# Kernel optimization log

Measured on AMD Instinct MI355X. Metric: run time of the kernel, lower is better.

The kernel has to match this reference:

```python
import jax, jax.numpy as jnp
import numpy as np

B, N, DH, DG, HID, K_STEPS, CURV = 256, 2048, 128, 256, 256, 2, 1.0
SC = CURV ** 0.5
SCALE = 1.0 / (DH ** 0.5)
LN_EPS = 1e-5


def _artanh(x):
    return jnp.arctanh(jnp.clip(x, -1.0 + 1e-5, 1.0 - 1e-5))


def logmap0(x, sc=SC):
    n = jnp.maximum(jnp.linalg.norm(x, axis=-1, keepdims=True), 1e-7)
    return x * (_artanh(sc * n) / (sc * n))


def expmap0(v, sc=SC):
    n = jnp.maximum(jnp.linalg.norm(v, axis=-1, keepdims=True), 1e-7)
    return v * (jnp.tanh(sc * n) / (sc * n))


def setup_inputs() -> dict:
    key = jax.random.key(0)
    ks = jax.random.split(key, 16)

    def lin(k, out_d, in_d):
        return (jax.random.normal(k, (out_d, in_d), jnp.float32) * (in_d ** -0.5))

    demo_hyp = expmap0(0.1 * jax.random.normal(ks[0], (B, N, DH), jnp.float32))
    rho_g = jax.random.normal(ks[1], (B, DG), jnp.float32)
    return {
        "demo_hyp": demo_hyp,
        "rho_g": rho_g,
        "seed_g_w": lin(ks[2], DH, DG),
        "seed_g_b": jnp.zeros((DH,), jnp.float32),
        "seed_d_w": lin(ks[3], DH, DH),
        "pool_wq_w": lin(ks[4], DH, DH),
        "pool_wk_w": lin(ks[5], DH, DH),
        "pool_wv_w": lin(ks[6], DH, DH),
        "q_u_w": lin(ks[7], DH, DH),
        "q_g_w": lin(ks[8], DH, DG),
        "q_g_b": jnp.zeros((DH,), jnp.float32),
        "kv_w": lin(ks[9], DH, DH),
        "mlp_w1": lin(ks[10], HID, DH),
        "mlp_b1": jnp.zeros((HID,), jnp.float32),
        "mlp_w2": lin(ks[11], DH, HID),
        "mlp_b2": jnp.zeros((DH,), jnp.float32),
        "ln_g": jnp.ones((DH,), jnp.float32),
        "ln_b": jnp.zeros((DH,), jnp.float32),
    }


def reference(demo_hyp, rho_g, seed_g_w, seed_g_b, seed_d_w,
              pool_wq_w, pool_wk_w, pool_wv_w, q_u_w, q_g_w, q_g_b,
              kv_w, mlp_w1, mlp_b1, mlp_w2, mlp_b2, ln_g, ln_b):
    demo_tan = logmap0(demo_hyp)                       # (B,N,Dh)

    # seed: attention-pool demos with rho_g query
    q_seed = rho_g @ seed_g_w.T + seed_g_b             # (B,Dh)
    qk = q_seed @ pool_wq_w.T                          # (B,Dh)
    Kp = demo_tan @ pool_wk_w.T                        # (B,N,Dh)
    a = jax.nn.softmax(jnp.einsum('bd,bnd->bn', qk, Kp) * SCALE, axis=-1)
    Vp = demo_tan @ pool_wv_w.T
    pooled = jnp.einsum('bn,bnd->bd', a, Vp)           # (B,Dh)
    u = expmap0(q_seed + pooled @ seed_d_w.T)

    for _ in range(K_STEPS):
        u_tan = logmap0(u)
        mu = jnp.mean(u_tan, axis=-1, keepdims=True)
        var = jnp.var(u_tan, axis=-1, keepdims=True)
        u_tan = (u_tan - mu) * jax.lax.rsqrt(var + LN_EPS) * ln_g + ln_b
        q = u_tan @ q_u_w.T + rho_g @ q_g_w.T + q_g_b
        Kmat = demo_tan @ kv_w.T                       # keys == values
        att = jax.nn.softmax(jnp.einsum('bd,bnd->bn', q, Kmat) * SCALE, axis=-1)
        delta = jnp.einsum('bn,bnd->bd', att, Kmat)
        upd = jax.nn.gelu(delta @ mlp_w1.T + mlp_b1, approximate=False) @ mlp_w2.T + mlp_b2
        u = expmap0(u_tan + upd)
    return u
```

## Files before the change

### kernel.cpp

```cpp
#include <hip/hip_runtime.h>
#include <cstddef>
#include <cstdint>

#define B 256
#define N 2048
#define DH 128
#define DG 256
#define HID 256
#define SPLITS 8
#define CHUNK (N / SPLITS)
#define KITER (CHUNK / 16)
#define SCALE 0.08838834764831845f
#define LN_EPS 1e-5f
#define TAN_NORM_MAX 6.2f


__device__ __forceinline__ float artanh_clip(float a) {
  a = fminf(a, 1.0f - 1e-5f);
  return 0.5f * __logf((1.0f + a) / (1.0f - a));
}

__device__ __forceinline__ float logmap_scale(float n2) {
  float nc = fmaxf(sqrtf(n2), 1e-7f);
  return artanh_clip(nc) / nc;
}

__device__ __forceinline__ float dotN(const float* __restrict__ wrow,
                                      const float* __restrict__ x, int n4) {
  const float4* a = (const float4*)wrow;
  const float4* bx = (const float4*)x;
  float s = 0.f;
  for (int j = 0; j < n4; ++j) {
    float4 u = a[j], v = bx[j];
    s += u.x * v.x + u.y * v.y + u.z * v.z + u.w * v.w;
  }
  return s;
}

__device__ __forceinline__ float blockSum128(float v, float* s_red) {
#pragma unroll
  for (int msk = 1; msk < 64; msk <<= 1) v += __shfl_xor(v, msk);
  if ((threadIdx.x & 63) == 0) s_red[threadIdx.x >> 6] = v;
  __syncthreads();
  float r = s_red[0] + s_red[1];
  __syncthreads();
  return r;
}

__device__ __forceinline__ float combine_partials(const float* __restrict__ partials,
                                                  int b, int tid) {
  const float* pb = partials + (size_t)b * SPLITS * (DH + 2);
  float L = 0.f, a = 0.f;
#pragma unroll
  for (int s = 0; s < SPLITS; ++s) {
    L += pb[s * (DH + 2) + DH];
    a += pb[s * (DH + 2) + tid];
  }
  return a / L;
}


__global__ void setup_pool_query(const float* __restrict__ rho,
                                 const float* __restrict__ seed_g_w,
                                 const float* __restrict__ seed_g_b,
                                 const float* __restrict__ pool_wq_w,
                                 const float* __restrict__ pool_wk_w,
                                 float* __restrict__ q_seed,
                                 float* __restrict__ qvec,
                                 float* __restrict__ mb) {
  const int b = blockIdx.x, tid = threadIdx.x;
  __shared__ __align__(16) float s_rho[DG];
  __shared__ __align__(16) float s_qs[DH];
  __shared__ __align__(16) float s_qk[DH];
  __shared__ float s_red[2];
  s_rho[tid] = rho[b * DG + tid];
  s_rho[tid + DH] = rho[b * DG + tid + DH];
  __syncthreads();
  float qs = seed_g_b[tid] + dotN(seed_g_w + (size_t)tid * DG, s_rho, DG / 4);
  q_seed[b * DH + tid] = qs;
  s_qs[tid] = qs;
  __syncthreads();
  float qk = dotN(pool_wq_w + (size_t)tid * DH, s_qs, DH / 4);
  s_qk[tid] = qk;
  __syncthreads();
  float qp = 0.f;
  for (int i = 0; i < DH; ++i) qp += pool_wk_w[i * DH + tid] * s_qk[i];
  qvec[b * DH + tid] = qp;
  float qn2 = blockSum128(qp * qp, s_red);
  if (tid == 0) mb[b] = SCALE * TAN_NORM_MAX * sqrtf(qn2);
}


__global__ __launch_bounds__(256, 6) void attn_pass(const float* __restrict__ demo,
                                                    const float* __restrict__ qvec,
                                                    const float* __restrict__ mb,
                                                    float* __restrict__ partials) {
  const int blk = blockIdx.x;
  const int b = blk >> 3;
  const int s = blk & 7;
  const int tid = threadIdx.x;
  const int w = tid >> 6;
  const int lane = tid & 63;
  const int il = lane & 31;
  const int half = lane >> 5;

  const float4 qv = *(const float4*)(qvec + b * DH + ((lane * 4) & 127));
  const float Mb = mb[b];
  const float* p0 = demo + ((size_t)b * N + (size_t)s * CHUNK + (size_t)(w * 2)) * DH + lane * 4;

  float la = 0.f, lb = 0.f;
  float4 aa = make_float4(0.f, 0.f, 0.f, 0.f);
  float4 ab = make_float4(0.f, 0.f, 0.f, 0.f);

  float4 xa = *(const float4*)(p0);
  float4 xb = *(const float4*)(p0 + 8 * DH);

  for (int k = 0; k < KITER; ++k) {
    float4 ca = xa, cb = xb;
    if (k + 1 < KITER) {
      const float* pn_ = p0 + (size_t)(k + 1) * 16 * DH;
      xa = *(const float4*)(pn_);
      xb = *(const float4*)(pn_ + 8 * DH);
    }
    {
      float n2 = ca.x * ca.x + ca.y * ca.y + ca.z * ca.z + ca.w * ca.w;
      float dd = qv.x * ca.x + qv.y * ca.y + qv.z * ca.z + qv.w * ca.w;
#pragma unroll
      for (int msk = 1; msk < 32; msk <<= 1) {
        n2 += __shfl_xor(n2, msk);
        dd += __shfl_xor(dd, msk);
      }
      float ts = logmap_scale(n2);
      float p = __expf(dd * ts * SCALE - Mb);
      la += p;
      float c = p * ts;
      aa.x += c * ca.x; aa.y += c * ca.y; aa.z += c * ca.z; aa.w += c * ca.w;
    }
    {
      float n2 = cb.x * cb.x + cb.y * cb.y + cb.z * cb.z + cb.w * cb.w;
      float dd = qv.x * cb.x + qv.y * cb.y + qv.z * cb.z + qv.w * cb.w;
#pragma unroll
      for (int msk = 1; msk < 32; msk <<= 1) {
        n2 += __shfl_xor(n2, msk);
        dd += __shfl_xor(dd, msk);
      }
      float ts = logmap_scale(n2);
      float p = __expf(dd * ts * SCALE - Mb);
      lb += p;
      float c = p * ts;
      ab.x += c * cb.x; ab.y += c * cb.y; ab.z += c * cb.z; ab.w += c * cb.w;
    }
  }

  float l = la + lb;
  float4 acc;
  acc.x = aa.x + ab.x; acc.y = aa.y + ab.y; acc.z = aa.z + ab.z; acc.w = aa.w + ab.w;
  acc.x += __shfl_xor(acc.x, 32);
  acc.y += __shfl_xor(acc.y, 32);
  acc.z += __shfl_xor(acc.z, 32);
  acc.w += __shfl_xor(acc.w, 32);
  l += __shfl_xor(l, 32);

  __shared__ __align__(16) float s_acc[4][DH];
  __shared__ float s_l[4];
  if (half == 0) *(float4*)&s_acc[w][il * 4] = acc;
  if (lane == 0) s_l[w] = l;
  __syncthreads();
  if (tid < DH) {
    float a = s_acc[0][tid] + s_acc[1][tid] + s_acc[2][tid] + s_acc[3][tid];
    float* p = partials + (size_t)blk * (DH + 2);
    p[tid] = a;
    if (tid == 0) p[DH] = s_l[0] + s_l[1] + s_l[2] + s_l[3];
  }
}


__global__ void trans_pool(const float* __restrict__ partials,
                           const float* __restrict__ q_seed,
                           const float* __restrict__ rho,
                           const float* __restrict__ pool_wv_w,
                           const float* __restrict__ seed_d_w,
                           const float* __restrict__ q_u_w,
                           const float* __restrict__ q_g_w,
                           const float* __restrict__ q_g_b,
                           const float* __restrict__ kv_w,
                           const float* __restrict__ ln_g,
                           const float* __restrict__ ln_b,
                           float* __restrict__ u_tan_out,
                           float* __restrict__ qvec_out,
                           float* __restrict__ mb) {
  const int b = blockIdx.x, tid = threadIdx.x;
  __shared__ __align__(16) float s_a[DH];
  __shared__ __align__(16) float s_b[DH];
  __shared__ __align__(16) float s_rho[DG];
  __shared__ float s_red[2];

  float w0 = combine_partials(partials, b, tid);
  s_a[tid] = w0;
  s_rho[tid] = rho[b * DG + tid];
  s_rho[tid + DH] = rho[b * DG + tid + DH];
  __syncthreads();
  float pooled = dotN(pool_wv_w + (size_t)tid * DH, s_a, DH / 4);
  s_b[tid] = pooled;
  __syncthreads();
  float v = q_seed[b * DH + tid] + dotN(seed_d_w + (size_t)tid * DH, s_b, DH / 4);
  float n2 = blockSum128(v * v, s_red);
  float nc = fmaxf(sqrtf(n2), 1e-7f);
  float u = v * (tanhf(nc) / nc);
  float nu2 = blockSum128(u * u, s_red);
  float nuc = fmaxf(sqrtf(nu2), 1e-7f);
  float ut = u * (artanh_clip(nuc) / nuc);
  float mu = blockSum128(ut, s_red) * (1.0f / DH);
  float d = ut - mu;
  float var = blockSum128(d * d, s_red) * (1.0f / DH);
  float y = d * rsqrtf(var + LN_EPS) * ln_g[tid] + ln_b[tid];
  u_tan_out[b * DH + tid] = y;
  s_a[tid] = y;
  __syncthreads();
  float q = q_g_b[tid] + dotN(q_u_w + (size_t)tid * DH, s_a, DH / 4) +
            dotN(q_g_w + (size_t)tid * DG, s_rho, DG / 4);
  s_b[tid] = q;
  __syncthreads();
  float qp = 0.f;
  for (int i = 0; i < DH; ++i) qp += kv_w[i * DH + tid] * s_b[i];
  qvec_out[b * DH + tid] = qp;
  float qn2 = blockSum128(qp * qp, s_red);
  if (tid == 0) mb[b] = SCALE * TAN_NORM_MAX * sqrtf(qn2);
}


__global__ void trans_iter(const float* __restrict__ partials,
                           const float* __restrict__ u_tan_in,
                           const float* __restrict__ rho,
                           const float* __restrict__ kv_w,
                           const float* __restrict__ mlp_w1,
                           const float* __restrict__ mlp_b1,
                           const float* __restrict__ mlp_w2,
                           const float* __restrict__ mlp_b2,
                           const float* __restrict__ q_u_w,
                           const float* __restrict__ q_g_w,
                           const float* __restrict__ q_g_b,
                           const float* __restrict__ ln_g,
                           const float* __restrict__ ln_b,
                           float* __restrict__ u_tan_out,
                           float* __restrict__ qvec_out,
                           float* __restrict__ mb,
                           float* __restrict__ out, int is_final) {
  const int b = blockIdx.x, tid = threadIdx.x;
  __shared__ __align__(16) float s_a[DH];
  __shared__ __align__(16) float s_b[DH];
  __shared__ __align__(16) float s_h[HID];
  __shared__ __align__(16) float s_rho[DG];
  __shared__ float s_red[2];

  float wv = combine_partials(partials, b, tid);
  s_a[tid] = wv;
  s_rho[tid] = rho[b * DG + tid];
  s_rho[tid + DH] = rho[b * DG + tid + DH];
  __syncthreads();
  float delta = dotN(kv_w + (size_t)tid * DH, s_a, DH / 4);
  s_b[tid] = delta;
  __syncthreads();
  float h0 = mlp_b1[tid] + dotN(mlp_w1 + (size_t)tid * DH, s_b, DH / 4);
  float h1 = mlp_b1[tid + DH] + dotN(mlp_w1 + (size_t)(tid + DH) * DH, s_b, DH / 4);
  s_h[tid] = 0.5f * h0 * (1.0f + erff(h0 * 0.70710678118654752f));
  s_h[tid + DH] = 0.5f * h1 * (1.0f + erff(h1 * 0.70710678118654752f));
  __syncthreads();
  float upd = mlp_b2[tid] + dotN(mlp_w2 + (size_t)tid * HID, s_h, HID / 4);
  float v = u_tan_in[b * DH + tid] + upd;
  float n2 = blockSum128(v * v, s_red);
  float nc = fmaxf(sqrtf(n2), 1e-7f);
  float u = v * (tanhf(nc) / nc);
  if (is_final) {
    out[b * DH + tid] = u;
    return;
  }
  float nu2 = blockSum128(u * u, s_red);
  float nuc = fmaxf(sqrtf(nu2), 1e-7f);
  float ut = u * (artanh_clip(nuc) / nuc);
  float mu = blockSum128(ut, s_red) * (1.0f / DH);
  float d = ut - mu;
  float var = blockSum128(d * d, s_red) * (1.0f / DH);
  float y = d * rsqrtf(var + LN_EPS) * ln_g[tid] + ln_b[tid];
  u_tan_out[b * DH + tid] = y;
  s_a[tid] = y;
  __syncthreads();
  float q = q_g_b[tid] + dotN(q_u_w + (size_t)tid * DH, s_a, DH / 4) +
            dotN(q_g_w + (size_t)tid * DG, s_rho, DG / 4);
  s_b[tid] = q;
  __syncthreads();
  float qp = 0.f;
  for (int i = 0; i < DH; ++i) qp += kv_w[i * DH + tid] * s_b[i];
  qvec_out[b * DH + tid] = qp;
  float qn2 = blockSum128(qp * qp, s_red);
  if (tid == 0) mb[b] = SCALE * TAN_NORM_MAX * sqrtf(qn2);
}


extern "C" void kernel_launch(void* const* d_in, const int* in_sizes, int n_in,
                              void* d_out, int out_size, void* d_ws, size_t ws_size,
                              hipStream_t stream) {
  const float* demo      = (const float*)d_in[0];
  const float* rho       = (const float*)d_in[1];
  const float* seed_g_w  = (const float*)d_in[2];
  const float* seed_g_b  = (const float*)d_in[3];
  const float* seed_d_w  = (const float*)d_in[4];
  const float* pool_wq_w = (const float*)d_in[5];
  const float* pool_wk_w = (const float*)d_in[6];
  const float* pool_wv_w = (const float*)d_in[7];
  const float* q_u_w     = (const float*)d_in[8];
  const float* q_g_w     = (const float*)d_in[9];
  const float* q_g_b     = (const float*)d_in[10];
  const float* kv_w      = (const float*)d_in[11];
  const float* mlp_w1    = (const float*)d_in[12];
  const float* mlp_b1    = (const float*)d_in[13];
  const float* mlp_w2    = (const float*)d_in[14];
  const float* mlp_b2    = (const float*)d_in[15];
  const float* ln_g      = (const float*)d_in[16];
  const float* ln_b      = (const float*)d_in[17];
  float* out = (float*)d_out;

  float* ws = (float*)d_ws;
  float* qvec  = ws;
  float* qseed = ws + B * DH;
  float* utanA = ws + 2 * B * DH;
  float* utanB = ws + 3 * B * DH;
  float* mb    = ws + 4 * B * DH;
  float* parts = ws + 4 * B * DH + B;

  setup_pool_query<<<B, DH, 0, stream>>>(rho, seed_g_w, seed_g_b, pool_wq_w,
                                         pool_wk_w, qseed, qvec, mb);
  attn_pass<<<B * SPLITS, 256, 0, stream>>>(demo, qvec, mb, parts);
  trans_pool<<<B, DH, 0, stream>>>(parts, qseed, rho, pool_wv_w, seed_d_w,
                                   q_u_w, q_g_w, q_g_b, kv_w, ln_g, ln_b,
                                   utanA, qvec, mb);
  attn_pass<<<B * SPLITS, 256, 0, stream>>>(demo, qvec, mb, parts);
  trans_iter<<<B, DH, 0, stream>>>(parts, utanA, rho, kv_w, mlp_w1, mlp_b1,
                                   mlp_w2, mlp_b2, q_u_w, q_g_w, q_g_b, ln_g,
                                   ln_b, utanB, qvec, mb, out, 0);
  attn_pass<<<B * SPLITS, 256, 0, stream>>>(demo, qvec, mb, parts);
  trans_iter<<<B, DH, 0, stream>>>(parts, utanB, rho, kv_w, mlp_w1, mlp_b1,
                                   mlp_w2, mlp_b2, q_u_w, q_g_w, q_g_b, ln_g,
                                   ln_b, utanB, qvec, mb, out, 1);
}
```

Measured before the change: 615.6 us.

## Cache per-row logmap scales and use DPP 16-lane row reductions in attention pass

New measurement: 602.8 us. -2.1%, faster.

```diff
diff --git a/kernel.cpp b/kernel.cpp
--- a/kernel.cpp
+++ b/kernel.cpp
@@ -9,7 +9,8 @@
 #define HID 256
 #define SPLITS 8
 #define CHUNK (N / SPLITS)
-#define KITER (CHUNK / 16)
+#define ROWS_PER_ITER 32
+#define KITER (CHUNK / ROWS_PER_ITER)
 #define SCALE 0.08838834764831845f
 #define LN_EPS 1e-5f
 #define TAN_NORM_MAX 6.2f
@@ -23,6 +24,14 @@
 __device__ __forceinline__ float logmap_scale(float n2) {
   float nc = fmaxf(sqrtf(n2), 1e-7f);
   return artanh_clip(nc) / nc;
+}
+
+__device__ __forceinline__ float row16_sum(float x) {
+  x += __int_as_float(__builtin_amdgcn_update_dpp(0, __float_as_int(x), 0x128, 0xF, 0xF, true));
+  x += __int_as_float(__builtin_amdgcn_update_dpp(0, __float_as_int(x), 0x124, 0xF, 0xF, true));
+  x += __int_as_float(__builtin_amdgcn_update_dpp(0, __float_as_int(x), 0x122, 0xF, 0xF, true));
+  x += __int_as_float(__builtin_amdgcn_update_dpp(0, __float_as_int(x), 0x121, 0xF, 0xF, true));
+  return x;
 }
 
 __device__ __forceinline__ float dotN(const float* __restrict__ wrow,
@@ -91,86 +100,115 @@
 }
 
 
+template <int LOADTS>
 __global__ __launch_bounds__(256, 6) void attn_pass(const float* __restrict__ demo,
                                                     const float* __restrict__ qvec,
                                                     const float* __restrict__ mb,
-                                                    float* __restrict__ partials) {
+                                                    float* __restrict__ partials,
+                                                    float* __restrict__ ts_buf) {
   const int blk = blockIdx.x;
   const int b = blk >> 3;
   const int s = blk & 7;
   const int tid = threadIdx.x;
   const int w = tid >> 6;
   const int lane = tid & 63;
-  const int il = lane & 31;
-  const int half = lane >> 5;
-
-  const float4 qv = *(const float4*)(qvec + b * DH + ((lane * 4) & 127));
+  const int g = lane >> 4;
+  const int il = lane & 15;
+
+  const float4 qv0 = *(const float4*)(qvec + b * DH + il * 4);
+  const float4 qv1 = *(const float4*)(qvec + b * DH + 64 + il * 4);
   const float Mb = mb[b];
-  const float* p0 = demo + ((size_t)b * N + (size_t)s * CHUNK + (size_t)(w * 2)) * DH + lane * 4;
-
-  float la = 0.f, lb = 0.f;
-  float4 aa = make_float4(0.f, 0.f, 0.f, 0.f);
-  float4 ab = make_float4(0.f, 0.f, 0.f, 0.f);
-
-  float4 xa = *(const float4*)(p0);
-  float4 xb = *(const float4*)(p0 + 8 * DH);
+
+  const size_t row0 = (size_t)b * N + (size_t)s * CHUNK + (size_t)(w * 8);
+  const float* p = demo + (row0 + g) * DH + il * 4;
+  const size_t rts = row0 + g;
+
+  float lsum = 0.f;
+  float4 accL = make_float4(0.f, 0.f, 0.f, 0.f);
+  float4 accH = make_float4(0.f, 0.f, 0.f, 0.f);
+
+  float4 xa1 = *(const float4*)(p);
+  float4 xa2 = *(const float4*)(p + 64);
+  float4 xb1 = *(const float4*)(p + 4 * DH);
+  float4 xb2 = *(const float4*)(p + 4 * DH + 64);
+  float tsA = 0.f, tsB = 0.f;
+  if (LOADTS) { tsA = ts_buf[rts]; tsB = ts_buf[rts + 4]; }
 
   for (int k = 0; k < KITER; ++k) {
-    float4 ca = xa, cb = xb;
+    float4 ca1 = xa1, ca2 = xa2, cb1 = xb1, cb2 = xb2;
+    float tA = tsA, tB = tsB;
     if (k + 1 < KITER) {
-      const float* pn_ = p0 + (size_t)(k + 1) * 16 * DH;
-      xa = *(const float4*)(pn_);
-      xb = *(const float4*)(pn_ + 8 * DH);
+      const float* pn = p + (size_t)(k + 1) * ROWS_PER_ITER * DH;
+      xa1 = *(const float4*)(pn);
+      xa2 = *(const float4*)(pn + 64);
+      xb1 = *(const float4*)(pn + 4 * DH);
+      xb2 = *(const float4*)(pn + 4 * DH + 64);
+      if (LOADTS) {
+        tsA = ts_buf[rts + (size_t)(k + 1) * ROWS_PER_ITER];
+        tsB = ts_buf[rts + (size_t)(k + 1) * ROWS_PER_ITER + 4];
+      }
     }
     {
-      float n2 = ca.x * ca.x + ca.y * ca.y + ca.z * ca.z + ca.w * ca.w;
-      float dd = qv.x * ca.x + qv.y * ca.y + qv.z * ca.z + qv.w * ca.w;
-#pragma unroll
-      for (int msk = 1; msk < 32; msk <<= 1) {
-        n2 += __shfl_xor(n2, msk);
-        dd += __shfl_xor(dd, msk);
+      float dd = qv0.x * ca1.x + qv0.y * ca1.y + qv0.z * ca1.z + qv0.w * ca1.w +
+                 qv1.x * ca2.x + qv1.y * ca2.y + qv1.z * ca2.z + qv1.w * ca2.w;
+      dd = row16_sum(dd);
+      float tsv;
+      if (LOADTS) {
+        tsv = tA;
+      } else {
+        float n2 = ca1.x * ca1.x + ca1.y * ca1.y + ca1.z * ca1.z + ca1.w * ca1.w +
+                   ca2.x * ca2.x + ca2.y * ca2.y + ca2.z * ca2.z + ca2.w * ca2.w;
+        n2 = row16_sum(n2);
+        tsv = logmap_scale(n2);
+        if (il == 0) ts_buf[rts + (size_t)k * ROWS_PER_ITER] = tsv;
       }
-      float ts = logmap_scale(n2);
-      float p = __expf(dd * ts * SCALE - Mb);
-      la += p;
-      float c = p * ts;
-      aa.x += c * ca.x; aa.y += c * ca.y; aa.z += c * ca.z; aa.w += c * ca.w;
+      float pw = __expf(dd * tsv * SCALE - Mb);
+      lsum += pw;
+      float c = pw * tsv;
+      accL.x += c * ca1.x; accL.y += c * ca1.y; accL.z += c * ca1.z; accL.w += c * ca1.w;
+      accH.x += c * ca2.x; accH.y += c * ca2.y; accH.z += c * ca2.z; accH.w += c * ca2.w;
     }
     {
-      float n2 = cb.x * cb.x + cb.y * cb.y + cb.z * cb.z + cb.w * cb.w;
-      float dd = qv.x * cb.x + qv.y * cb.y + qv.z * cb.z + qv.w * cb.w;
+      float dd = qv0.x * cb1.x + qv0.y * cb1.y + qv0.z * cb1.z + qv0.w * cb1.w +
+                 qv1.x * cb2.x + qv1.y * cb2.y + qv1.z * cb2.z + qv1.w * cb2.w;
+      dd = row16_sum(dd);
+      float tsv;
+      if (LOADTS) {
+        tsv = tB;
+      } else {
+        float n2 = cb1.x * cb1.x + cb1.y * cb1.y + cb1.z * cb1.z + cb1.w * cb1.w +
+                   cb2.x * cb2.x + cb2.y * cb2.y + cb2.z * cb2.z + cb2.w * cb2.w;
+        n2 = row16_sum(n2);
+        tsv = logmap_scale(n2);
+        if (il == 0) ts_buf[rts + (size_t)k * ROWS_PER_ITER + 4] = tsv;
+      }
+      float pw = __expf(dd * tsv * SCALE - Mb);
+      lsum += pw;
+      float c = pw * tsv;
+      accL.x += c * cb1.x; accL.y += c * cb1.y; accL.z += c * cb1.z; accL.w += c * cb1.w;
+      accH.x += c * cb2.x; accH.y += c * cb2.y; accH.z += c * cb2.z; accH.w += c * cb2.w;
+    }
+  }
+
+  __shared__ __align__(16) float s_acc[16][DH];
+  __shared__ float s_l[16];
+  const int slot = (w << 2) | g;
+  *(float4*)&s_acc[slot][il * 4] = accL;
+  *(float4*)&s_acc[slot][64 + il * 4] = accH;
+  if (il == 0) s_l[slot] = lsum;
+  __syncthreads();
+  if (tid < DH) {
+    float a = 0.f;
 #pragma unroll
-      for (int msk = 1; msk < 32; msk <<= 1) {
-        n2 += __shfl_xor(n2, msk);
-        dd += __shfl_xor(dd, msk);
-      }
-      float ts = logmap_scale(n2);
-      float p = __expf(dd * ts * SCALE - Mb);
-      lb += p;
-      float c = p * ts;
-      ab.x += c * cb.x; ab.y += c * cb.y; ab.z += c * cb.z; ab.w += c * cb.w;
+    for (int j = 0; j < 16; ++j) a += s_acc[j][tid];
+    float* pp = partials + (size_t)blk * (DH + 2);
+    pp[tid] = a;
+    if (tid == 0) {
+      float L = 0.f;
+#pragma unroll
+      for (int j = 0; j < 16; ++j) L += s_l[j];
+      pp[DH] = L;
     }
-  }
-
-  float l = la + lb;
-  float4 acc;
-  acc.x = aa.x + ab.x; acc.y = aa.y + ab.y; acc.z = aa.z + ab.z; acc.w = aa.w + ab.w;
-  acc.x += __shfl_xor(acc.x, 32);
-  acc.y += __shfl_xor(acc.y, 32);
-  acc.z += __shfl_xor(acc.z, 32);
-  acc.w += __shfl_xor(acc.w, 32);
-  l += __shfl_xor(l, 32);
-
-  __shared__ __align__(16) float s_acc[4][DH];
-  __shared__ float s_l[4];
-  if (half == 0) *(float4*)&s_acc[w][il * 4] = acc;
-  if (lane == 0) s_l[w] = l;
-  __syncthreads();
-  if (tid < DH) {
-    float a = s_acc[0][tid] + s_acc[1][tid] + s_acc[2][tid] + s_acc[3][tid];
-    float* p = partials + (size_t)blk * (DH + 2);
-    p[tid] = a;
-    if (tid == 0) p[DH] = s_l[0] + s_l[1] + s_l[2] + s_l[3];
   }
 }
 
@@ -327,18 +365,19 @@
   float* utanB = ws + 3 * B * DH;
   float* mb    = ws + 4 * B * DH;
   float* parts = ws + 4 * B * DH + B;
+  float* tsbuf = parts + B * SPLITS * (DH + 2);
 
   setup_pool_query<<<B, DH, 0, stream>>>(rho, seed_g_w, seed_g_b, pool_wq_w,
                                          pool_wk_w, qseed, qvec, mb);
-  attn_pass<<<B * SPLITS, 256, 0, stream>>>(demo, qvec, mb, parts);
+  attn_pass<0><<<B * SPLITS, 256, 0, stream>>>(demo, qvec, mb, parts, tsbuf);
   trans_pool<<<B, DH, 0, stream>>>(parts, qseed, rho, pool_wv_w, seed_d_w,
                                    q_u_w, q_g_w, q_g_b, kv_w, ln_g, ln_b,
                                    utanA, qvec, mb);
-  attn_pass<<<B * SPLITS, 256, 0, stream>>>(demo, qvec, mb, parts);
+  attn_pass<1><<<B * SPLITS, 256, 0, stream>>>(demo, qvec, mb, parts, tsbuf);
   trans_iter<<<B, DH, 0, stream>>>(parts, utanA, rho, kv_w, mlp_w1, mlp_b1,
                                    mlp_w2, mlp_b2, q_u_w, q_g_w, q_g_b, ln_g,
                                    ln_b, utanB, qvec, mb, out, 0);
-  attn_pass<<<B * SPLITS, 256, 0, stream>>>(demo, qvec, mb, parts);
+  attn_pass<1><<<B * SPLITS, 256, 0, stream>>>(demo, qvec, mb, parts, tsbuf);
   trans_iter<<<B, DH, 0, stream>>>(parts, utanB, rho, kv_w, mlp_w1, mlp_b1,
                                    mlp_w2, mlp_b2, q_u_w, q_g_w, q_g_b, ln_g,
                                    ln_b, utanB, qvec, mb, out, 1);
```
